# Kernel tuning notes

Measured on AMD Instinct MI355X. Metric: run time of the kernel, lower is better.

Reference implementation:

```python
import jax, jax.numpy as jnp
import numpy as np

TY = 10  # decoder loop uses the global Ty=10 in the original code


def _bi_lstm_dir(X, Wih, Whh, b, n_hidden):
    # X: (m, T, F); returns hidden states (m, T, n_hidden). Gate order: i,f,g,o.
    m = X.shape[0]
    def step(carry, x_t):
        h, c = carry
        g = x_t @ Wih.T + h @ Whh.T + b
        i, f, gg, o = jnp.split(g, 4, axis=-1)
        c = jax.nn.sigmoid(f) * c + jax.nn.sigmoid(i) * jnp.tanh(gg)
        h = jax.nn.sigmoid(o) * jnp.tanh(c)
        return (h, c), h
    h0 = jnp.zeros((m, n_hidden), X.dtype)
    _, hs = jax.lax.scan(step, (h0, h0), jnp.swapaxes(X, 0, 1))
    return jnp.swapaxes(hs, 0, 1)


def setup_inputs() -> dict:
    key = jax.random.key(0)
    ks = jax.random.split(key, 17)
    m, Tx, F = 256, 256, 128
    n_a, n_s, vocab, attn_h = 256, 512, 1024, 10
    def w(k, shape, fan_in):
        return (jax.random.normal(k, shape, jnp.float32) / np.sqrt(fan_in)).astype(jnp.float32)
    return {
        "X": jax.random.normal(ks[0], (m, Tx, F), jnp.float32),
        "Wih_f": w(ks[1], (4 * n_a, F), F),
        "Whh_f": w(ks[2], (4 * n_a, n_a), n_a),
        "b_f": w(ks[3], (4 * n_a,), n_a),
        "Wih_b": w(ks[4], (4 * n_a, F), F),
        "Whh_b": w(ks[5], (4 * n_a, n_a), n_a),
        "b_b": w(ks[6], (4 * n_a,), n_a),
        "W1": w(ks[7], (attn_h, 2 * n_a + n_s), 2 * n_a + n_s),
        "b1": w(ks[8], (attn_h,), attn_h),
        "W2": w(ks[9], (1, attn_h), attn_h),
        "b2": w(ks[10], (1,), attn_h),
        "Wc_ih": w(ks[11], (4 * n_s, n_s), n_s),
        "Wc_hh": w(ks[12], (4 * n_s, n_s), n_s),
        "bc": w(ks[13], (4 * n_s,), n_s),
        "Wfc": w(ks[14], (vocab, n_s), n_s),
        "bfc": w(ks[15], (vocab,), n_s),
    }


def reference(X, Wih_f, Whh_f, b_f, Wih_b, Whh_b, b_b, W1, b1, W2, b2, Wc_ih, Wc_hh, bc, Wfc, bfc):
    m, Tx, _ = X.shape
    n_a = Whh_f.shape[1]
    n_s = Wc_hh.shape[1]
    # bidirectional encoder
    a_f = _bi_lstm_dir(X, Wih_f, Whh_f, b_f, n_a)
    a_b = _bi_lstm_dir(X[:, ::-1], Wih_b, Whh_b, b_b, n_a)[:, ::-1]
    a = jnp.concatenate([a_f, a_b], axis=-1)  # (m, Tx, 2*n_a)
    # decoder: initial h_n = zeros(m, 2, n_a).flatten(1) == zeros(m, n_s) since n_s = 2*n_a
    s = jnp.zeros((m, n_s), X.dtype)
    c = jnp.zeros((m, n_s), X.dtype)
    outs = []
    for _ in range(TY):
        sp = jnp.broadcast_to(s[:, None, :], (m, Tx, n_s))
        concat = jnp.concatenate([a, sp], axis=-1)           # (m, Tx, 2*n_a + n_s)
        e = jnp.tanh(concat @ W1.T + b1)                     # (m, Tx, 10)
        scores = jax.nn.relu(e @ W2.T + b2)                  # (m, Tx, 1)
        alphas = jax.nn.softmax(scores, axis=1)              # softmax over Tx
        context = jnp.sum(alphas * a, axis=1)                # (m, 2*n_a) == (m, n_s)
        g = context @ Wc_ih.T + s @ Wc_hh.T + bc             # LSTMCell
        i, f, gg, o = jnp.split(g, 4, axis=-1)
        c = jax.nn.sigmoid(f) * c + jax.nn.sigmoid(i) * jnp.tanh(gg)
        s = jax.nn.sigmoid(o) * jnp.tanh(c)
        outs.append(s @ Wfc.T + bfc)                         # (m, vocab)
    return jnp.stack(outs, axis=1)                           # (m, Ty, vocab)
```

## Files before the change

kernel.cpp:

```cpp
#include <hip/hip_runtime.h>
#include <hip/hip_bf16.h>
#include <hip/hip_cooperative_groups.h>

namespace cg = cooperative_groups;

#define TXN 256
#define NA 256
#define NF 128
#define NS 512
#define TYN 10
#define VOCAB 1024

#define A_STR 392
#define W_STR 392
#define WL_OFF (64 * W_STR)
#define AH_OFF (2 * 64 * W_STR)
#define AL_OFF (AH_OFF + 32 * A_STR)
#define PRE_OFF_US (AL_OFF + 32 * A_STR)
#define ENC_LDS_BYTES (150528 + 32 * 68 * 4 + 64 * 4)

#define D_STR 264
#define D_WH 0
#define D_WL (64 * D_STR)
#define D_AH (2 * 64 * D_STR)
#define D_AL (D_AH + 32 * D_STR)
#define D_PRE_US (D_AL + 32 * D_STR)
#define DEC_LDS_BYTES (101376 + 32 * 68 * 4 + 64 * 4)

typedef __attribute__((ext_vector_type(8))) short bf16x8;
typedef __attribute__((ext_vector_type(4))) float f32x4;

__device__ __forceinline__ float fsigmoid(float x) { return 1.f / (1.f + __expf(-x)); }
__device__ __forceinline__ float ftanh(float x)    { return 1.f - 2.f / (1.f + __expf(2.f * x)); }

__device__ __forceinline__ void split_bf16(float v, unsigned short& hi, unsigned short& lo) {
    __hip_bfloat16 h = __float2bfloat16(v);
    float rem = v - __bfloat162float(h);
    __hip_bfloat16 l = __float2bfloat16(rem);
    hi = *reinterpret_cast<unsigned short*>(&h);
    lo = *reinterpret_cast<unsigned short*>(&l);
}

__global__ __launch_bounds__(256, 1) void encoder_kernel(
    const float* __restrict__ X,
    const float* __restrict__ Wih_f, const float* __restrict__ Whh_f, const float* __restrict__ b_f,
    const float* __restrict__ Wih_b, const float* __restrict__ Whh_b, const float* __restrict__ b_b,
    float* __restrict__ a, unsigned int* __restrict__ bar)
{
    extern __shared__ unsigned char smem_raw[];
    unsigned short* Wh  = (unsigned short*)smem_raw;
    unsigned short* Wl  = (unsigned short*)smem_raw + WL_OFF;
    unsigned short* Ahh = (unsigned short*)smem_raw + AH_OFF;
    unsigned short* All = (unsigned short*)smem_raw + AL_OFF;
    float* Pre = (float*)(smem_raw + (size_t)PRE_OFF_US * 2);
    float* bsh = Pre + 32 * 68;

    const int tid = threadIdx.x;
    const int dir = blockIdx.x & 1;
    const int bid = blockIdx.x >> 1;
    const int i0 = (bid >> 4) * 32;
    const int j0 = (bid & 15) * 16;
    const int grp = dir * 8 + (bid >> 4);
    const int myjb = bid & 15;
    unsigned int* slots = bar + grp * 16;

    const float* __restrict__ Wih = dir ? Wih_b : Wih_f;
    const float* __restrict__ Whh = dir ? Whh_b : Whh_f;
    const float* __restrict__ bv  = dir ? b_b  : b_f;

    const int jl = tid & 15;
    const int ip = tid >> 4;
    const int iA = ip * 2;

    if (tid < 64) bsh[tid] = bv[(tid >> 4) * NA + j0 + (tid & 15)];
    for (int r = 0; r < 64; ++r) {
        int row = (r >> 4) * NA + j0 + (r & 15);
        unsigned short hi, lo;
        split_bf16(Whh[(size_t)row * NA + tid], hi, lo);
        Wh[r * W_STR + tid] = hi;
        Wl[r * W_STR + tid] = lo;
        if (tid < NF) {
            split_bf16(Wih[(size_t)row * NF + tid], hi, lo);
            Wh[r * W_STR + 256 + tid] = hi;
            Wl[r * W_STR + 256 + tid] = lo;
        }
    }

    #pragma unroll 4
    for (int r = 0; r < 32; ++r) {
        Ahh[r * A_STR + tid] = 0;
        All[r * A_STR + tid] = 0;
    }
    {
        const int t0 = dir ? (TXN - 1) : 0;
        const int kx = tid & 127;
        const int rbase = tid >> 7;
        #pragma unroll 4
        for (int rr = 0; rr < 16; ++rr) {
            int r = rr * 2 + rbase;
            float v = X[((size_t)(i0 + r) * TXN + t0) * NF + kx];
            unsigned short hi, lo;
            split_bf16(v, hi, lo);
            Ahh[r * A_STR + 256 + kx] = hi;
            All[r * A_STR + 256 + kx] = lo;
        }
    }

    float c0 = 0.f, c1 = 0.f;

    const int lane = tid & 63;
    const int wv   = tid >> 6;
    const int rt   = wv >> 1;
    const int g0   = (wv & 1) * 2;
    const int ln   = lane & 15;
    const int quad = lane >> 4;
    const unsigned short* pAh = Ahh + (rt * 16 + ln) * A_STR + quad * 8;
    const unsigned short* pAl = All + (rt * 16 + ln) * A_STR + quad * 8;
    const unsigned short* pW0h = Wh + (g0 * 16 + ln) * W_STR + quad * 8;
    const unsigned short* pW0l = Wl + (g0 * 16 + ln) * W_STR + quad * 8;
    const unsigned short* pW1h = pW0h + 16 * W_STR;
    const unsigned short* pW1l = pW0l + 16 * W_STR;

    for (int step = 0; step < TXN; ++step) {
        const int t = dir ? (TXN - 1 - step) : step;

        if (step != 0) {
            const int tprev = dir ? (t + 1) : (t - 1);
            const int jb = tid >> 4;
            while (__hip_atomic_load(&slots[jb], __ATOMIC_RELAXED,
                                     __HIP_MEMORY_SCOPE_AGENT) < (unsigned)step) {}
            float hv[32];
            #pragma unroll
            for (int r = 0; r < 32; ++r) {
                hv[r] = __hip_atomic_load(
                    &a[(((size_t)(i0 + r) * TXN + tprev) << 9) + dir * NA + tid],
                    __ATOMIC_RELAXED, __HIP_MEMORY_SCOPE_AGENT);
            }
            #pragma unroll
            for (int r = 0; r < 32; ++r) {
                unsigned short hi, lo;
                split_bf16(hv[r], hi, lo);
                Ahh[r * A_STR + tid] = hi;
                All[r * A_STR + tid] = lo;
            }
        }
        __syncthreads();

        f32x4 a0e = {0.f,0.f,0.f,0.f}, a0o = {0.f,0.f,0.f,0.f};
        f32x4 a1e = {0.f,0.f,0.f,0.f}, a1o = {0.f,0.f,0.f,0.f};
        #pragma unroll
        for (int kp = 0; kp < 6; ++kp) {
            {
                const int kc = kp * 2;
                bf16x8 fah = *(const bf16x8*)(pAh + kc * 32);
                bf16x8 fal = *(const bf16x8*)(pAl + kc * 32);
                bf16x8 w0h = *(const bf16x8*)(pW0h + kc * 32);
                bf16x8 w0l = *(const bf16x8*)(pW0l + kc * 32);
                bf16x8 w1h = *(const bf16x8*)(pW1h + kc * 32);
                bf16x8 w1l = *(const bf16x8*)(pW1l + kc * 32);
                a0e = __builtin_amdgcn_mfma_f32_16x16x32_bf16(fal, w0h, a0e, 0, 0, 0);
                a0e = __builtin_amdgcn_mfma_f32_16x16x32_bf16(fah, w0l, a0e, 0, 0, 0);
                a0e = __builtin_amdgcn_mfma_f32_16x16x32_bf16(fah, w0h, a0e, 0, 0, 0);
                a1e = __builtin_amdgcn_mfma_f32_16x16x32_bf16(fal, w1h, a1e, 0, 0, 0);
                a1e = __builtin_amdgcn_mfma_f32_16x16x32_bf16(fah, w1l, a1e, 0, 0, 0);
                a1e = __builtin_amdgcn_mfma_f32_16x16x32_bf16(fah, w1h, a1e, 0, 0, 0);
            }
            {
                const int kc = kp * 2 + 1;
                bf16x8 fah = *(const bf16x8*)(pAh + kc * 32);
                bf16x8 fal = *(const bf16x8*)(pAl + kc * 32);
                bf16x8 w0h = *(const bf16x8*)(pW0h + kc * 32);
                bf16x8 w0l = *(const bf16x8*)(pW0l + kc * 32);
                bf16x8 w1h = *(const bf16x8*)(pW1h + kc * 32);
                bf16x8 w1l = *(const bf16x8*)(pW1l + kc * 32);
                a0o = __builtin_amdgcn_mfma_f32_16x16x32_bf16(fal, w0h, a0o, 0, 0, 0);
                a0o = __builtin_amdgcn_mfma_f32_16x16x32_bf16(fah, w0l, a0o, 0, 0, 0);
                a0o = __builtin_amdgcn_mfma_f32_16x16x32_bf16(fah, w0h, a0o, 0, 0, 0);
                a1o = __builtin_amdgcn_mfma_f32_16x16x32_bf16(fal, w1h, a1o, 0, 0, 0);
                a1o = __builtin_amdgcn_mfma_f32_16x16x32_bf16(fah, w1l, a1o, 0, 0, 0);
                a1o = __builtin_amdgcn_mfma_f32_16x16x32_bf16(fah, w1h, a1o, 0, 0, 0);
            }
        }
        #pragma unroll
        for (int reg = 0; reg < 4; ++reg) {
            int prow = rt * 16 + quad * 4 + reg;
            Pre[prow * 68 + g0 * 16 + ln]       = a0e[reg] + a0o[reg];
            Pre[prow * 68 + (g0 + 1) * 16 + ln] = a1e[reg] + a1o[reg];
        }
        __syncthreads();

        float h0, h1;
        {
            float gi = fsigmoid(Pre[iA * 68 +      jl] + bsh[jl]);
            float gf = fsigmoid(Pre[iA * 68 + 16 + jl] + bsh[16 + jl]);
            float gg = ftanh  (Pre[iA * 68 + 32 + jl] + bsh[32 + jl]);
            float go = fsigmoid(Pre[iA * 68 + 48 + jl] + bsh[48 + jl]);
            c0 = gf * c0 + gi * gg;
            h0 = go * ftanh(c0);
        }
        {
            float gi = fsigmoid(Pre[(iA + 1) * 68 +      jl] + bsh[jl]);
            float gf = fsigmoid(Pre[(iA + 1) * 68 + 16 + jl] + bsh[16 + jl]);
            float gg = ftanh  (Pre[(iA + 1) * 68 + 32 + jl] + bsh[32 + jl]);
            float go = fsigmoid(Pre[(iA + 1) * 68 + 48 + jl] + bsh[48 + jl]);
            c1 = gf * c1 + gi * gg;
            h1 = go * ftanh(c1);
        }
        __hip_atomic_store(
            &a[(((size_t)(i0 + iA)     * TXN + t) << 9) + dir * NA + j0 + jl],
            h0, __ATOMIC_RELAXED, __HIP_MEMORY_SCOPE_AGENT);
        __hip_atomic_store(
            &a[(((size_t)(i0 + iA + 1) * TXN + t) << 9) + dir * NA + j0 + jl],
            h1, __ATOMIC_RELAXED, __HIP_MEMORY_SCOPE_AGENT);

        if (step != TXN - 1) {
            __syncthreads();
            if (tid == 0) {
                __hip_atomic_store(&slots[myjb], (unsigned)(step + 1),
                                   __ATOMIC_RELAXED, __HIP_MEMORY_SCOPE_AGENT);
            }
            {
                const int tn = dir ? (t - 1) : (t + 1);
                const int kx = tid & 127;
                const int rbase = tid >> 7;
                #pragma unroll 4
                for (int rr = 0; rr < 16; ++rr) {
                    int r = rr * 2 + rbase;
                    float v = X[((size_t)(i0 + r) * TXN + tn) * NF + kx];
                    unsigned short hi, lo;
                    split_bf16(v, hi, lo);
                    Ahh[r * A_STR + 256 + kx] = hi;
                    All[r * A_STR + 256 + kx] = lo;
                }
            }
        }
    }
}

__global__ __launch_bounds__(256) void wsplit_cat(
    const float* __restrict__ Wc_ih, const float* __restrict__ Wc_hh,
    unsigned short* __restrict__ Wh, unsigned short* __restrict__ Wl)
{
    int idx = blockIdx.x * 256 + threadIdx.x;
    int r = idx >> 10, k = idx & 1023;
    float v = (k < 512) ? Wc_ih[(size_t)r * 512 + k] : Wc_hh[(size_t)r * 512 + (k - 512)];
    unsigned short hi, lo;
    split_bf16(v, hi, lo);
    Wh[idx] = hi; Wl[idx] = lo;
}

__global__ __launch_bounds__(256) void wsplit_fc(
    const float* __restrict__ Wfc,
    unsigned short* __restrict__ Wh, unsigned short* __restrict__ Wl)
{
    int idx = blockIdx.x * 256 + threadIdx.x;
    unsigned short hi, lo;
    split_bf16(Wfc[idx], hi, lo);
    Wh[idx] = hi; Wl[idx] = lo;
}

__global__ __launch_bounds__(256, 1) void gates_kernel(
    const float* __restrict__ xcat,
    const unsigned short* __restrict__ Wch,
    const unsigned short* __restrict__ Wcl,
    const float* __restrict__ bc,
    float* __restrict__ c_buf,
    float* __restrict__ s_buf,
    float* __restrict__ xc_out)
{
    extern __shared__ unsigned char smem_raw[];
    unsigned short* Wh = (unsigned short*)smem_raw + D_WH;
    unsigned short* Wl = (unsigned short*)smem_raw + D_WL;
    unsigned short* Ah = (unsigned short*)smem_raw + D_AH;
    unsigned short* Al = (unsigned short*)smem_raw + D_AL;
    float* Pre = (float*)(smem_raw + (size_t)D_PRE_US * 2);
    float* bsh = Pre + 32 * 68;

    const int tid = threadIdx.x;
    const int i0 = blockIdx.x * 32;
    const int j0 = blockIdx.y * 16;

    if (tid < 64) bsh[tid] = bc[(tid >> 4) * 512 + j0 + (tid & 15)];

    const int lane = tid & 63;
    const int wv   = tid >> 6;
    const int rt   = wv >> 1;
    const int g0   = (wv & 1) * 2;
    const int ln   = lane & 15;
    const int quad = lane >> 4;
    const unsigned short* pAh = Ah + (rt * 16 + ln) * D_STR + quad * 8;
    const unsigned short* pAl = Al + (rt * 16 + ln) * D_STR + quad * 8;
    const unsigned short* pW0h = Wh + (g0 * 16 + ln) * D_STR + quad * 8;
    const unsigned short* pW0l = Wl + (g0 * 16 + ln) * D_STR + quad * 8;
    const unsigned short* pW1h = pW0h + 16 * D_STR;
    const unsigned short* pW1l = pW0l + 16 * D_STR;

    const int rW = tid >> 2;
    const int qW = (tid & 3) * 64;
    const int rowg = (rW >> 4) * 512 + j0 + (rW & 15);

    f32x4 a0 = {0.f,0.f,0.f,0.f}, a1 = {0.f,0.f,0.f,0.f};

    for (int ch = 0; ch < 4; ++ch) {
        const int kc0 = ch * 256;
        __syncthreads();
        #pragma unroll 8
        for (int r = 0; r < 32; ++r) {
            float v = xcat[(size_t)(i0 + r) * 1024 + kc0 + tid];
            unsigned short hi, lo;
            split_bf16(v, hi, lo);
            Ah[r * D_STR + tid] = hi;
            Al[r * D_STR + tid] = lo;
        }
        {
            const size_t base = (size_t)rowg * 1024 + kc0 + qW;
            #pragma unroll
            for (int i = 0; i < 8; ++i) {
                *(bf16x8*)&Wh[rW * D_STR + qW + i * 8] = *(const bf16x8*)&Wch[base + i * 8];
                *(bf16x8*)&Wl[rW * D_STR + qW + i * 8] = *(const bf16x8*)&Wcl[base + i * 8];
            }
        }
        __syncthreads();
        #pragma unroll
        for (int kc = 0; kc < 8; ++kc) {
            bf16x8 fah = *(const bf16x8*)(pAh + kc * 32);
            bf16x8 fal = *(const bf16x8*)(pAl + kc * 32);
            bf16x8 w0h = *(const bf16x8*)(pW0h + kc * 32);
            bf16x8 w0l = *(const bf16x8*)(pW0l + kc * 32);
            bf16x8 w1h = *(const bf16x8*)(pW1h + kc * 32);
            bf16x8 w1l = *(const bf16x8*)(pW1l + kc * 32);
            a0 = __builtin_amdgcn_mfma_f32_16x16x32_bf16(fal, w0h, a0, 0, 0, 0);
            a0 = __builtin_amdgcn_mfma_f32_16x16x32_bf16(fah, w0l, a0, 0, 0, 0);
            a0 = __builtin_amdgcn_mfma_f32_16x16x32_bf16(fah, w0h, a0, 0, 0, 0);
            a1 = __builtin_amdgcn_mfma_f32_16x16x32_bf16(fal, w1h, a1, 0, 0, 0);
            a1 = __builtin_amdgcn_mfma_f32_16x16x32_bf16(fah, w1l, a1, 0, 0, 0);
            a1 = __builtin_amdgcn_mfma_f32_16x16x32_bf16(fah, w1h, a1, 0, 0, 0);
        }
    }
    #pragma unroll
    for (int reg = 0; reg < 4; ++reg) {
        int prow = rt * 16 + quad * 4 + reg;
        Pre[prow * 68 + g0 * 16 + ln]       = a0[reg];
        Pre[prow * 68 + (g0 + 1) * 16 + ln] = a1[reg];
    }
    __syncthreads();

    const int jl = tid & 15;
    const int iA = (tid >> 4) * 2;
    #pragma unroll
    for (int rr = 0; rr < 2; ++rr) {
        int r = iA + rr;
        float gi = fsigmoid(Pre[r * 68 +      jl] + bsh[jl]);
        float gf = fsigmoid(Pre[r * 68 + 16 + jl] + bsh[16 + jl]);
        float gg = ftanh  (Pre[r * 68 + 32 + jl] + bsh[32 + jl]);
        float go = fsigmoid(Pre[r * 68 + 48 + jl] + bsh[48 + jl]);
        size_t ci = (size_t)(i0 + r) * 512 + j0 + jl;
        float cn = gf * c_buf[ci] + gi * gg;
        c_buf[ci] = cn;
        float h = go * ftanh(cn);
        s_buf[ci] = h;
        xc_out[(size_t)(i0 + r) * 1024 + 512 + j0 + jl] = h;
    }
}

__global__ __launch_bounds__(256, 1) void logits_kernel(
    const float* __restrict__ s_buf,
    const unsigned short* __restrict__ Wfh,
    const unsigned short* __restrict__ Wfl,
    const float* __restrict__ bfc,
    float* __restrict__ out, int ty)
{
    extern __shared__ unsigned char smem_raw[];
    unsigned short* Wh = (unsigned short*)smem_raw + D_WH;
    unsigned short* Wl = (unsigned short*)smem_raw + D_WL;
    unsigned short* Ah = (unsigned short*)smem_raw + D_AH;
    unsigned short* Al = (unsigned short*)smem_raw + D_AL;

    const int tid = threadIdx.x;
    const int i0 = blockIdx.x * 32;
    const int v0 = blockIdx.y * 64;

    const int lane = tid & 63;
    const int wv   = tid >> 6;
    const int rt   = wv >> 1;
    const int ct   = wv & 1;
    const int ln   = lane & 15;
    const int quad = lane >> 4;
    const unsigned short* pAh = Ah + (rt * 16 + ln) * D_STR + quad * 8;
    const unsigned short* pAl = Al + (rt * 16 + ln) * D_STR + quad * 8;
    const unsigned short* pW0h = Wh + (ct * 32 + ln) * D_STR + quad * 8;
    const unsigned short* pW0l = Wl + (ct * 32 + ln) * D_STR + quad * 8;
    const unsigned short* pW1h = pW0h + 16 * D_STR;
    const unsigned short* pW1l = pW0l + 16 * D_STR;

    const int rW = tid >> 2;
    const int qW = (tid & 3) * 64;

    f32x4 a0 = {0.f,0.f,0.f,0.f}, a1 = {0.f,0.f,0.f,0.f};

    for (int ch = 0; ch < 2; ++ch) {
        const int kc0 = ch * 256;
        __syncthreads();
        #pragma unroll 8
        for (int r = 0; r < 32; ++r) {
            float v = s_buf[(size_t)(i0 + r) * 512 + kc0 + tid];
            unsigned short hi, lo;
            split_bf16(v, hi, lo);
            Ah[r * D_STR + tid] = hi;
            Al[r * D_STR + tid] = lo;
        }
        {
            const size_t base = (size_t)(v0 + rW) * 512 + kc0 + qW;
            #pragma unroll
            for (int i = 0; i < 8; ++i) {
                *(bf16x8*)&Wh[rW * D_STR + qW + i * 8] = *(const bf16x8*)&Wfh[base + i * 8];
                *(bf16x8*)&Wl[rW * D_STR + qW + i * 8] = *(const bf16x8*)&Wfl[base + i * 8];
            }
        }
        __syncthreads();
        #pragma unroll
        for (int kc = 0; kc < 8; ++kc) {
            bf16x8 fah = *(const bf16x8*)(pAh + kc * 32);
            bf16x8 fal = *(const bf16x8*)(pAl + kc * 32);
            bf16x8 w0h = *(const bf16x8*)(pW0h + kc * 32);
            bf16x8 w0l = *(const bf16x8*)(pW0l + kc * 32);
            bf16x8 w1h = *(const bf16x8*)(pW1h + kc * 32);
            bf16x8 w1l = *(const bf16x8*)(pW1l + kc * 32);
            a0 = __builtin_amdgcn_mfma_f32_16x16x32_bf16(fal, w0h, a0, 0, 0, 0);
            a0 = __builtin_amdgcn_mfma_f32_16x16x32_bf16(fah, w0l, a0, 0, 0, 0);
            a0 = __builtin_amdgcn_mfma_f32_16x16x32_bf16(fah, w0h, a0, 0, 0, 0);
            a1 = __builtin_amdgcn_mfma_f32_16x16x32_bf16(fal, w1h, a1, 0, 0, 0);
            a1 = __builtin_amdgcn_mfma_f32_16x16x32_bf16(fah, w1l, a1, 0, 0, 0);
            a1 = __builtin_amdgcn_mfma_f32_16x16x32_bf16(fah, w1h, a1, 0, 0, 0);
        }
    }
    #pragma unroll
    for (int reg = 0; reg < 4; ++reg) {
        int row = i0 + rt * 16 + quad * 4 + reg;
        int col0 = v0 + ct * 32 + ln;
        out[(size_t)row * (TYN * VOCAB) + ty * VOCAB + col0]      = a0[reg] + bfc[col0];
        out[(size_t)row * (TYN * VOCAB) + ty * VOCAB + col0 + 16] = a1[reg] + bfc[col0 + 16];
    }
}

__global__ __launch_bounds__(256) void attn_prep(
    const float* __restrict__ a, const float* __restrict__ W1,
    const float* __restrict__ b1, float* __restrict__ aW1)
{
    __shared__ float Wsh[10][516];
    __shared__ float red[64][10][4];
    const int tid = threadIdx.x;
    for (int idx = tid; idx < 10 * 512; idx += 256) {
        int o = idx >> 9, k = idx & 511;
        Wsh[o][k] = W1[o * 1024 + k];
    }
    __syncthreads();
    const int r = tid >> 2, kq = tid & 3;
    const float* ar = a + ((size_t)blockIdx.x * 64 + r) * 512 + kq * 128;
    float acc[10] = {};
    for (int k = 0; k < 128; k += 4) {
        float4 v = *(const float4*)&ar[k];
        #pragma unroll
        for (int o = 0; o < 10; ++o) {
            float4 w = *(const float4*)&Wsh[o][kq * 128 + k];
            acc[o] += v.x * w.x + v.y * w.y + v.z * w.z + v.w * w.w;
        }
    }
    #pragma unroll
    for (int o = 0; o < 10; ++o) red[r][o][kq] = acc[o];
    __syncthreads();
    for (int idx = tid; idx < 640; idx += 256) {
        int rr = idx / 10, o = idx % 10;
        float s = red[rr][o][0] + red[rr][o][1] + red[rr][o][2] + red[rr][o][3] + b1[o];
        aW1[((size_t)blockIdx.x * 64 + rr) * 10 + o] = s;
    }
}

__global__ __launch_bounds__(256) void attn_kernel(
    const float* __restrict__ aW1,
    const float* __restrict__ s_buf,
    const float* __restrict__ W1,
    const float* __restrict__ W2,
    const float* __restrict__ b2,
    const float* __restrict__ a,
    float* __restrict__ xcat)
{
    __shared__ float sh_s[10];
    __shared__ float sh_w2[10];
    __shared__ float sred[160];
    __shared__ float red[256];
    __shared__ float al[256];
    __shared__ float4 ctxred[256];
    const int i = blockIdx.x;
    const int tid = threadIdx.x;

    if (tid < 160) {
        int o = tid >> 4, part = tid & 15;
        const float* srow = s_buf + (size_t)i * 512;
        const float* wrow = W1 + o * 1024 + 512;
        float p = 0.f;
        for (int k = part; k < 512; k += 16) p += srow[k] * wrow[k];
        sred[tid] = p;
    }
    __syncthreads();
    if (tid < 10) {
        float v = 0.f;
        #pragma unroll
        for (int p = 0; p < 16; ++p) v += sred[tid * 16 + p];
        sh_s[tid] = v;
        sh_w2[tid] = W2[tid];
    }
    __syncthreads();

    float sum = b2[0];
    const float* ar = aW1 + ((size_t)i * TXN + tid) * 10;
    #pragma unroll
    for (int h = 0; h < 10; ++h) {
        float e = ftanh(ar[h] + sh_s[h]);
        sum += e * sh_w2[h];
    }
    float sc = fmaxf(sum, 0.f);

    red[tid] = sc;
    __syncthreads();
    for (int s = 128; s > 0; s >>= 1) {
        if (tid < s) red[tid] = fmaxf(red[tid], red[tid + s]);
        __syncthreads();
    }
    float mx = red[0];
    __syncthreads();
    float p = __expf(sc - mx);
    red[tid] = p;
    __syncthreads();
    for (int s = 128; s > 0; s >>= 1) {
        if (tid < s) red[tid] += red[tid + s];
        __syncthreads();
    }
    float inv = 1.f / red[0];
    al[tid] = p * inv;
    __syncthreads();

    const int half = tid >> 7;
    const int q    = tid & 127;
    const float* abase = a + (size_t)i * TXN * NS + q * 4;
    float4 acc = make_float4(0.f, 0.f, 0.f, 0.f);
    #pragma unroll 8
    for (int t = half; t < TXN; t += 2) {
        float w = al[t];
        float4 v = *(const float4*)&abase[(size_t)t * NS];
        acc.x += w * v.x; acc.y += w * v.y; acc.z += w * v.z; acc.w += w * v.w;
    }
    ctxred[tid] = acc;
    __syncthreads();
    if (tid < 128) {
        float4 e = ctxred[tid];
        float4 o = ctxred[tid + 128];
        float4 r4 = make_float4(e.x + o.x, e.y + o.y, e.z + o.z, e.w + o.w);
        *(float4*)&xcat[(size_t)i * 1024 + tid * 4] = r4;
    }
}

extern "C" void kernel_launch(void* const* d_in, const int* in_sizes, int n_in,
                              void* d_out, int out_size, void* d_ws, size_t ws_size,
                              hipStream_t stream)
{
    const float* X     = (const float*)d_in[0];
    const float* Wih_f = (const float*)d_in[1];
    const float* Whh_f = (const float*)d_in[2];
    const float* b_f   = (const float*)d_in[3];
    const float* Wih_b = (const float*)d_in[4];
    const float* Whh_b = (const float*)d_in[5];
    const float* b_b   = (const float*)d_in[6];
    const float* W1    = (const float*)d_in[7];
    const float* b1    = (const float*)d_in[8];
    const float* W2    = (const float*)d_in[9];
    const float* b2    = (const float*)d_in[10];
    const float* Wc_ih = (const float*)d_in[11];
    const float* Wc_hh = (const float*)d_in[12];
    const float* bc    = (const float*)d_in[13];
    const float* Wfc   = (const float*)d_in[14];
    const float* bfc   = (const float*)d_in[15];
    float* out = (float*)d_out;
    float* ws  = (float*)d_ws;

    float* c_buf = ws;
    float* s_buf = ws + 131072;
    float* xcat  = ws + 262144;
    float* a     = ws + 524288;
    float* aW1   = ws + 34078720;
    unsigned short* Wch = (unsigned short*)(ws + 34734080);
    unsigned short* Wcl = (unsigned short*)(ws + 35782656);
    unsigned short* Wfh = (unsigned short*)(ws + 36831232);
    unsigned short* Wfl = (unsigned short*)(ws + 37093376);
    unsigned int* bar = (unsigned int*)(ws + 37358080);

    static int attrs_set = 0;
    if (!attrs_set) {
        hipFuncSetAttribute(reinterpret_cast<const void*>(encoder_kernel),
                            hipFuncAttributeMaxDynamicSharedMemorySize, ENC_LDS_BYTES);
        hipFuncSetAttribute(reinterpret_cast<const void*>(gates_kernel),
                            hipFuncAttributeMaxDynamicSharedMemorySize, DEC_LDS_BYTES);
        hipFuncSetAttribute(reinterpret_cast<const void*>(logits_kernel),
                            hipFuncAttributeMaxDynamicSharedMemorySize, DEC_LDS_BYTES);
        attrs_set = 1;
    }

    hipMemsetAsync(c_buf, 0, (size_t)524288 * sizeof(float), stream);
    hipMemsetAsync(bar, 0, 16 * 16 * sizeof(unsigned int), stream);

    wsplit_cat<<<8192, 256, 0, stream>>>(Wc_ih, Wc_hh, Wch, Wcl);
    wsplit_fc<<<2048, 256, 0, stream>>>(Wfc, Wfh, Wfl);

    {
        void* args[] = { (void*)&X, (void*)&Wih_f, (void*)&Whh_f, (void*)&b_f,
                         (void*)&Wih_b, (void*)&Whh_b, (void*)&b_b, (void*)&a, (void*)&bar };
        hipLaunchCooperativeKernel(reinterpret_cast<void*>(encoder_kernel),
                                   dim3(256), dim3(256), args, ENC_LDS_BYTES, stream);
    }

    attn_prep<<<1024, 256, 0, stream>>>(a, W1, b1, aW1);

    for (int ty = 0; ty < TYN; ++ty) {
        attn_kernel<<<256, 256, 0, stream>>>(aW1, s_buf, W1, W2, b2, a, xcat);
        gates_kernel<<<dim3(8, 32), 256, DEC_LDS_BYTES, stream>>>(
            xcat, Wch, Wcl, bc, c_buf, s_buf, xcat);
        logits_kernel<<<dim3(8, 16), 256, DEC_LDS_BYTES, stream>>>(
            s_buf, Wfh, Wfl, bfc, out, ty);
    }
}
```

Baseline: 2.194 ms.

## Defer decoder logits into one batched GEMM over all time steps

Decoder hidden states for all ten steps are stored in a combined buffer, and a single logits launch with a grid ten times larger replaces the ten small per-step launches. The gates kernel now reads the previous state directly rather than through a concatenated xcat copy, and ping-pong state buffers are used when the workspace is too small to hold every step. This removes per-step launch and serialization overhead on the logits path and fills more compute units. The cost is extra workspace and an added synchronization in the gates kernel.

After: 2.140 ms. -2.5%, faster.

```diff
diff --git a/kernel.cpp b/kernel.cpp
--- a/kernel.cpp
+++ b/kernel.cpp
@@ -39,6 +39,19 @@
     __hip_bfloat16 l = __float2bfloat16(rem);
     hi = *reinterpret_cast<unsigned short*>(&h);
     lo = *reinterpret_cast<unsigned short*>(&l);
+}
+
+__device__ __forceinline__ float agent_ld(const float* p) {
+    return __hip_atomic_load(p, __ATOMIC_RELAXED, __HIP_MEMORY_SCOPE_AGENT);
+}
+__device__ __forceinline__ void agent_st(float* p, float v) {
+    __hip_atomic_store(p, v, __ATOMIC_RELAXED, __HIP_MEMORY_SCOPE_AGENT);
+}
+__device__ __forceinline__ unsigned flag_ld(const unsigned* p) {
+    return __hip_atomic_load(p, __ATOMIC_RELAXED, __HIP_MEMORY_SCOPE_AGENT);
+}
+__device__ __forceinline__ void flag_st(unsigned* p, unsigned v) {
+    __hip_atomic_store(p, v, __ATOMIC_RELAXED, __HIP_MEMORY_SCOPE_AGENT);
 }
 
 __global__ __launch_bounds__(256, 1) void encoder_kernel(
@@ -127,14 +140,11 @@
         if (step != 0) {
             const int tprev = dir ? (t + 1) : (t - 1);
             const int jb = tid >> 4;
-            while (__hip_atomic_load(&slots[jb], __ATOMIC_RELAXED,
-                                     __HIP_MEMORY_SCOPE_AGENT) < (unsigned)step) {}
+            while (flag_ld(&slots[jb]) < (unsigned)step) {}
             float hv[32];
             #pragma unroll
             for (int r = 0; r < 32; ++r) {
-                hv[r] = __hip_atomic_load(
-                    &a[(((size_t)(i0 + r) * TXN + tprev) << 9) + dir * NA + tid],
-                    __ATOMIC_RELAXED, __HIP_MEMORY_SCOPE_AGENT);
+                hv[r] = agent_ld(&a[(((size_t)(i0 + r) * TXN + tprev) << 9) + dir * NA + tid]);
             }
             #pragma unroll
             for (int r = 0; r < 32; ++r) {
@@ -206,19 +216,12 @@
             c1 = gf * c1 + gi * gg;
             h1 = go * ftanh(c1);
         }
-        __hip_atomic_store(
-            &a[(((size_t)(i0 + iA)     * TXN + t) << 9) + dir * NA + j0 + jl],
-            h0, __ATOMIC_RELAXED, __HIP_MEMORY_SCOPE_AGENT);
-        __hip_atomic_store(
-            &a[(((size_t)(i0 + iA + 1) * TXN + t) << 9) + dir * NA + j0 + jl],
-            h1, __ATOMIC_RELAXED, __HIP_MEMORY_SCOPE_AGENT);
+        agent_st(&a[(((size_t)(i0 + iA)     * TXN + t) << 9) + dir * NA + j0 + jl], h0);
+        agent_st(&a[(((size_t)(i0 + iA + 1) * TXN + t) << 9) + dir * NA + j0 + jl], h1);
 
         if (step != TXN - 1) {
             __syncthreads();
-            if (tid == 0) {
-                __hip_atomic_store(&slots[myjb], (unsigned)(step + 1),
-                                   __ATOMIC_RELAXED, __HIP_MEMORY_SCOPE_AGENT);
-            }
+            if (tid == 0) flag_st(&slots[myjb], (unsigned)(step + 1));
             {
                 const int tn = dir ? (t - 1) : (t + 1);
                 const int kx = tid & 127;
@@ -259,14 +262,131 @@
     Wh[idx] = hi; Wl[idx] = lo;
 }
 
+__global__ __launch_bounds__(256) void attn_prep(
+    const float* __restrict__ a, const float* __restrict__ W1,
+    const float* __restrict__ b1, float* __restrict__ aW1)
+{
+    __shared__ float Wsh[10][516];
+    __shared__ float red[64][10][4];
+    const int tid = threadIdx.x;
+    for (int idx = tid; idx < 10 * 512; idx += 256) {
+        int o = idx >> 9, k = idx & 511;
+        Wsh[o][k] = W1[o * 1024 + k];
+    }
+    __syncthreads();
+    const int r = tid >> 2, kq = tid & 3;
+    const float* ar = a + ((size_t)blockIdx.x * 64 + r) * 512 + kq * 128;
+    float acc[10] = {};
+    for (int k = 0; k < 128; k += 4) {
+        float4 v = *(const float4*)&ar[k];
+        #pragma unroll
+        for (int o = 0; o < 10; ++o) {
+            float4 w = *(const float4*)&Wsh[o][kq * 128 + k];
+            acc[o] += v.x * w.x + v.y * w.y + v.z * w.z + v.w * w.w;
+        }
+    }
+    #pragma unroll
+    for (int o = 0; o < 10; ++o) red[r][o][kq] = acc[o];
+    __syncthreads();
+    for (int idx = tid; idx < 640; idx += 256) {
+        int rr = idx / 10, o = idx % 10;
+        float s = red[rr][o][0] + red[rr][o][1] + red[rr][o][2] + red[rr][o][3] + b1[o];
+        aW1[((size_t)blockIdx.x * 64 + rr) * 10 + o] = s;
+    }
+}
+
+__global__ __launch_bounds__(256) void attn_kernel(
+    const float* __restrict__ aW1,
+    const float* __restrict__ s_prev, int sp_stride,
+    const float* __restrict__ W1,
+    const float* __restrict__ W2,
+    const float* __restrict__ b2,
+    const float* __restrict__ a,
+    float* __restrict__ xcat)
+{
+    __shared__ float sh_s[10];
+    __shared__ float sh_w2[10];
+    __shared__ float sred[160];
+    __shared__ float red[256];
+    __shared__ float al[256];
+    __shared__ float4 ctxred[256];
+    const int i = blockIdx.x;
+    const int tid = threadIdx.x;
+
+    if (tid < 160) {
+        int o = tid >> 4, part = tid & 15;
+        const float* srow = s_prev + (size_t)i * sp_stride;
+        const float* wrow = W1 + o * 1024 + 512;
+        float p = 0.f;
+        for (int k = part; k < 512; k += 16) p += srow[k] * wrow[k];
+        sred[tid] = p;
+    }
+    __syncthreads();
+    if (tid < 10) {
+        float v = 0.f;
+        #pragma unroll
+        for (int p = 0; p < 16; ++p) v += sred[tid * 16 + p];
+        sh_s[tid] = v;
+        sh_w2[tid] = W2[tid];
+    }
+    __syncthreads();
+
+    float sum = b2[0];
+    const float* ar = aW1 + ((size_t)i * TXN + tid) * 10;
+    #pragma unroll
+    for (int h = 0; h < 10; ++h) {
+        float e = ftanh(ar[h] + sh_s[h]);
+        sum += e * sh_w2[h];
+    }
+    float sc = fmaxf(sum, 0.f);
+
+    red[tid] = sc;
+    __syncthreads();
+    for (int s = 128; s > 0; s >>= 1) {
+        if (tid < s) red[tid] = fmaxf(red[tid], red[tid + s]);
+        __syncthreads();
+    }
+    float mx = red[0];
+    __syncthreads();
+    float p = __expf(sc - mx);
+    red[tid] = p;
+    __syncthreads();
+    for (int s = 128; s > 0; s >>= 1) {
+        if (tid < s) red[tid] += red[tid + s];
+        __syncthreads();
+    }
+    float inv = 1.f / red[0];
+    al[tid] = p * inv;
+    __syncthreads();
+
+    const int half = tid >> 7;
+    const int q    = tid & 127;
+    const float* abase = a + (size_t)i * TXN * NS + q * 4;
+    float4 acc = make_float4(0.f, 0.f, 0.f, 0.f);
+    #pragma unroll 8
+    for (int t = half; t < TXN; t += 2) {
+        float w = al[t];
+        float4 v = *(const float4*)&abase[(size_t)t * NS];
+        acc.x += w * v.x; acc.y += w * v.y; acc.z += w * v.z; acc.w += w * v.w;
+    }
+    ctxred[tid] = acc;
+    __syncthreads();
+    if (tid < 128) {
+        float4 e = ctxred[tid];
+        float4 o = ctxred[tid + 128];
+        float4 r4 = make_float4(e.x + o.x, e.y + o.y, e.z + o.z, e.w + o.w);
+        *(float4*)&xcat[(size_t)i * 512 + tid * 4] = r4;
+    }
+}
+
 __global__ __launch_bounds__(256, 1) void gates_kernel(
     const float* __restrict__ xcat,
+    const float* __restrict__ s_prev, int sp_stride,
     const unsigned short* __restrict__ Wch,
     const unsigned short* __restrict__ Wcl,
     const float* __restrict__ bc,
     float* __restrict__ c_buf,
-    float* __restrict__ s_buf,
-    float* __restrict__ xc_out)
+    float* __restrict__ s_out, int so_stride)
 {
     extern __shared__ unsigned char smem_raw[];
     unsigned short* Wh = (unsigned short*)smem_raw + D_WH;
@@ -306,7 +426,9 @@
         __syncthreads();
         #pragma unroll 8
         for (int r = 0; r < 32; ++r) {
-            float v = xcat[(size_t)(i0 + r) * 1024 + kc0 + tid];
+            float v;
+            if (ch < 2) v = xcat[(size_t)(i0 + r) * 512 + kc0 + tid];
+            else        v = s_prev[(size_t)(i0 + r) * sp_stride + (kc0 - 512) + tid];
             unsigned short hi, lo;
             split_bf16(v, hi, lo);
             Ah[r * D_STR + tid] = hi;
@@ -337,6 +459,7 @@
             a1 = __builtin_amdgcn_mfma_f32_16x16x32_bf16(fah, w1h, a1, 0, 0, 0);
         }
     }
+    __syncthreads();
     #pragma unroll
     for (int reg = 0; reg < 4; ++reg) {
         int prow = rt * 16 + quad * 4 + reg;
@@ -357,18 +480,16 @@
         size_t ci = (size_t)(i0 + r) * 512 + j0 + jl;
         float cn = gf * c_buf[ci] + gi * gg;
         c_buf[ci] = cn;
-        float h = go * ftanh(cn);
-        s_buf[ci] = h;
-        xc_out[(size_t)(i0 + r) * 1024 + 512 + j0 + jl] = h;
+        s_out[(size_t)(i0 + r) * so_stride + j0 + jl] = go * ftanh(cn);
     }
 }
 
 __global__ __launch_bounds__(256, 1) void logits_kernel(
-    const float* __restrict__ s_buf,
+    const float* __restrict__ S, int s_stride,
     const unsigned short* __restrict__ Wfh,
     const unsigned short* __restrict__ Wfl,
     const float* __restrict__ bfc,
-    float* __restrict__ out, int ty)
+    float* __restrict__ out, int o_stride, int o_off)
 {
     extern __shared__ unsigned char smem_raw[];
     unsigned short* Wh = (unsigned short*)smem_raw + D_WH;
@@ -403,7 +524,7 @@
         __syncthreads();
         #pragma unroll 8
         for (int r = 0; r < 32; ++r) {
-            float v = s_buf[(size_t)(i0 + r) * 512 + kc0 + tid];
+            float v = S[(size_t)(i0 + r) * s_stride + kc0 + tid];
             unsigned short hi, lo;
             split_bf16(v, hi, lo);
             Ah[r * D_STR + tid] = hi;
@@ -438,125 +559,8 @@
     for (int reg = 0; reg < 4; ++reg) {
         int row = i0 + rt * 16 + quad * 4 + reg;
         int col0 = v0 + ct * 32 + ln;
-        out[(size_t)row * (TYN * VOCAB) + ty * VOCAB + col0]      = a0[reg] + bfc[col0];
-        out[(size_t)row * (TYN * VOCAB) + ty * VOCAB + col0 + 16] = a1[reg] + bfc[col0 + 16];
-    }
-}
-
-__global__ __launch_bounds__(256) void attn_prep(
-    const float* __restrict__ a, const float* __restrict__ W1,
-    const float* __restrict__ b1, float* __restrict__ aW1)
-{
-    __shared__ float Wsh[10][516];
-    __shared__ float red[64][10][4];
-    const int tid = threadIdx.x;
-    for (int idx = tid; idx < 10 * 512; idx += 256) {
-        int o = idx >> 9, k = idx & 511;
-        Wsh[o][k] = W1[o * 1024 + k];
-    }
-    __syncthreads();
-    const int r = tid >> 2, kq = tid & 3;
-    const float* ar = a + ((size_t)blockIdx.x * 64 + r) * 512 + kq * 128;
-    float acc[10] = {};
-    for (int k = 0; k < 128; k += 4) {
-        float4 v = *(const float4*)&ar[k];
-        #pragma unroll
-        for (int o = 0; o < 10; ++o) {
-            float4 w = *(const float4*)&Wsh[o][kq * 128 + k];
-            acc[o] += v.x * w.x + v.y * w.y + v.z * w.z + v.w * w.w;
-        }
-    }
-    #pragma unroll
-    for (int o = 0; o < 10; ++o) red[r][o][kq] = acc[o];
-    __syncthreads();
-    for (int idx = tid; idx < 640; idx += 256) {
-        int rr = idx / 10, o = idx % 10;
-        float s = red[rr][o][0] + red[rr][o][1] + red[rr][o][2] + red[rr][o][3] + b1[o];
-        aW1[((size_t)blockIdx.x * 64 + rr) * 10 + o] = s;
-    }
-}
-
-__global__ __launch_bounds__(256) void attn_kernel(
-    const float* __restrict__ aW1,
-    const float* __restrict__ s_buf,
-    const float* __restrict__ W1,
-    const float* __restrict__ W2,
-    const float* __restrict__ b2,
-    const float* __restrict__ a,
-    float* __restrict__ xcat)
-{
-    __shared__ float sh_s[10];
-    __shared__ float sh_w2[10];
-    __shared__ float sred[160];
-    __shared__ float red[256];
-    __shared__ float al[256];
-    __shared__ float4 ctxred[256];
-    const int i = blockIdx.x;
-    const int tid = threadIdx.x;
-
-    if (tid < 160) {
-        int o = tid >> 4, part = tid & 15;
-        const float* srow = s_buf + (size_t)i * 512;
-        const float* wrow = W1 + o * 1024 + 512;
-        float p = 0.f;
-        for (int k = part; k < 512; k += 16) p += srow[k] * wrow[k];
-        sred[tid] = p;
-    }
-    __syncthreads();
-    if (tid < 10) {
-        float v = 0.f;
-        #pragma unroll
-        for (int p = 0; p < 16; ++p) v += sred[tid * 16 + p];
-        sh_s[tid] = v;
-        sh_w2[tid] = W2[tid];
-    }
-    __syncthreads();
-
-    float sum = b2[0];
-    const float* ar = aW1 + ((size_t)i * TXN + tid) * 10;
-    #pragma unroll
-    for (int h = 0; h < 10; ++h) {
-        float e = ftanh(ar[h] + sh_s[h]);
-        sum += e * sh_w2[h];
-    }
-    float sc = fmaxf(sum, 0.f);
-
-    red[tid] = sc;
-    __syncthreads();
-    for (int s = 128; s > 0; s >>= 1) {
-        if (tid < s) red[tid] = fmaxf(red[tid], red[tid + s]);
-        __syncthreads();
-    }
-    float mx = red[0];
-    __syncthreads();
-    float p = __expf(sc - mx);
-    red[tid] = p;
-    __syncthreads();
-    for (int s = 128; s > 0; s >>= 1) {
-        if (tid < s) red[tid] += red[tid + s];
-        __syncthreads();
-    }
-    float inv = 1.f / red[0];
-    al[tid] = p * inv;
-    __syncthreads();
-
-    const int half = tid >> 7;
-    const int q    = tid & 127;
-    const float* abase = a + (size_t)i * TXN * NS + q * 4;
-    float4 acc = make_float4(0.f, 0.f, 0.f, 0.f);
-    #pragma unroll 8
-    for (int t = half; t < TXN; t += 2) {
-        float w = al[t];
-        float4 v = *(const float4*)&abase[(size_t)t * NS];
-        acc.x += w * v.x; acc.y += w * v.y; acc.z += w * v.z; acc.w += w * v.w;
-    }
-    ctxred[tid] = acc;
-    __syncthreads();
-    if (tid < 128) {
-        float4 e = ctxred[tid];
-        float4 o = ctxred[tid + 128];
-        float4 r4 = make_float4(e.x + o.x, e.y + o.y, e.z + o.z, e.w + o.w);
-        *(float4*)&xcat[(size_t)i * 1024 + tid * 4] = r4;
+        out[(size_t)row * o_stride + o_off + col0]      = a0[reg] + bfc[col0];
+        out[(size_t)row * o_stride + o_off + col0 + 16] = a1[reg] + bfc[col0 + 16];
     }
 }
 
@@ -584,15 +588,18 @@
     float* ws  = (float*)d_ws;
 
     float* c_buf = ws;
-    float* s_buf = ws + 131072;
-    float* xcat  = ws + 262144;
+    float* zbuf  = ws + 131072;
+    float* sbufB = ws + 262144;
+    float* xcat  = ws + 393216;
     float* a     = ws + 524288;
     float* aW1   = ws + 34078720;
     unsigned short* Wch = (unsigned short*)(ws + 34734080);
     unsigned short* Wcl = (unsigned short*)(ws + 35782656);
     unsigned short* Wfh = (unsigned short*)(ws + 36831232);
     unsigned short* Wfl = (unsigned short*)(ws + 37093376);
-    unsigned int* bar = (unsigned int*)(ws + 37358080);
+    unsigned int* bar   = (unsigned int*)(ws + 37355520);
+    float* S_all = ws + 37355776;
+    const int deferred = (ws_size >= (size_t)38666496 * sizeof(float)) ? 1 : 0;
 
     static int attrs_set = 0;
     if (!attrs_set) {
@@ -605,8 +612,8 @@
         attrs_set = 1;
     }
 
-    hipMemsetAsync(c_buf, 0, (size_t)524288 * sizeof(float), stream);
-    hipMemsetAsync(bar, 0, 16 * 16 * sizeof(unsigned int), stream);
+    hipMemsetAsync(c_buf, 0, (size_t)262144 * sizeof(float), stream);
+    hipMemsetAsync(bar, 0, 256 * sizeof(unsigned int), stream);
 
     wsplit_cat<<<8192, 256, 0, stream>>>(Wc_ih, Wc_hh, Wch, Wcl);
     wsplit_fc<<<2048, 256, 0, stream>>>(Wfc, Wfh, Wfl);
@@ -621,10 +628,24 @@
     attn_prep<<<1024, 256, 0, stream>>>(a, W1, b1, aW1);
 
     for (int ty = 0; ty < TYN; ++ty) {
-        attn_kernel<<<256, 256, 0, stream>>>(aW1, s_buf, W1, W2, b2, a, xcat);
+        const float* sprev; int spstr;
+        float* sout; int sostr;
+        if (ty == 0) { sprev = zbuf; spstr = 512; }
+        else if (deferred) { sprev = S_all + (size_t)(ty - 1) * 512; spstr = TYN * 512; }
+        else { sprev = (ty & 1) ? sbufB : zbuf; spstr = 512; }
+        if (deferred) { sout = S_all + (size_t)ty * 512; sostr = TYN * 512; }
+        else { sout = (ty & 1) ? zbuf : sbufB; sostr = 512; }
+
+        attn_kernel<<<256, 256, 0, stream>>>(aW1, sprev, spstr, W1, W2, b2, a, xcat);
         gates_kernel<<<dim3(8, 32), 256, DEC_LDS_BYTES, stream>>>(
-            xcat, Wch, Wcl, bc, c_buf, s_buf, xcat);
-        logits_kernel<<<dim3(8, 16), 256, DEC_LDS_BYTES, stream>>>(
-            s_buf, Wfh, Wfl, bfc, out, ty);
-    }
-}
+            xcat, sprev, spstr, Wch, Wcl, bc, c_buf, sout, sostr);
+        if (!deferred) {
+            logits_kernel<<<dim3(8, 16), 256, DEC_LDS_BYTES, stream>>>(
+                sout, 512, Wfh, Wfl, bfc, out, TYN * VOCAB, ty * VOCAB);
+        }
+    }
+    if (deferred) {
+        logits_kernel<<<dim3(80, 16), 256, DEC_LDS_BYTES, stream>>>(
+            S_all, 512, Wfh, Wfl, bfc, out, VOCAB, 0);
+    }
+}
```
